# Optimization experiments

Measured on AMD Instinct MI355X. Metric: run time of the kernel, lower is better.

## Reference

```python
import jax, jax.numpy as jnp
import numpy as np

N = 6144
IN_DIM = 512
CHANNELS = 4
C_DIM = 64
ITERATIONS = 3
BETA = 1.0
EDGE_P = 0.005  # ~30 avg degree


def _l2norm(x):
    # F.normalize(dim=-1): x / max(||x||_2, eps)
    return x / jnp.maximum(jnp.linalg.norm(x, axis=-1, keepdims=True), 1e-12)


def setup_inputs() -> dict:
    key = jax.random.key(0)
    kf, ka, kw, kb = jax.random.split(key, 4)
    features = jax.random.normal(kf, (N, IN_DIM), dtype=jnp.float32)
    # sparse 0/1 adjacency, densified (module calls adj.to_dense())
    adj = (jax.random.uniform(ka, (N, N)) < EDGE_P).astype(jnp.int32)
    # per-channel weights/biases, init ~ N(0, 1) as in init_parameters
    W = jax.random.normal(kw, (CHANNELS, IN_DIM, C_DIM), dtype=jnp.float32)
    b = jax.random.normal(kb, (CHANNELS, 1, C_DIM), dtype=jnp.float32)
    return {"features": features, "adj": adj, "W": W, "b": b}


def reference(features, adj, W, b):
    mask = adj > 0  # [N, N]
    # per-channel projection + row L2-normalize -> [C, N, K]
    feats = _l2norm(jnp.einsum('nd,cdk->cnk', features, W) + b)
    for _ in range(ITERATIONS):
        # per-channel dense self-attention scores, masked by adjacency
        att = jnp.einsum('cnk,cmk->cnm', feats, feats) / BETA  # [C, N, N]
        att = jnp.where(mask[None, :, :], att, 0.0)
        # softmax across channels (torch dim=2 after cat == channel axis)
        att = jax.nn.softmax(att, axis=0)
        att = jnp.where(mask[None, :, :], att, 0.0)
        # aggregate and renormalize
        feats = _l2norm(feats + jnp.einsum('cnm,cmk->cnk', att, feats))
    # concat channels along feature dim -> [N, C*K]
    return jnp.transpose(feats, (1, 0, 2)).reshape(N, CHANNELS * C_DIM)
```

## Files before the change

### kernel.cpp

```cpp
#include <hip/hip_runtime.h>
#include <hip/hip_bf16.h>
#include <math.h>

#define NN      6144
#define IN_DIM  512
#define CH      4
#define CDIM    64
#define NODE    (CH * CDIM)
#define PR      16
#define MAXD    96

__global__ __launch_bounds__(256) void proj_kernel(
    const float* __restrict__ feat,
    const float* __restrict__ W,
    const float* __restrict__ bias,
    float* __restrict__ out)
{
    __shared__ float lds[PR * IN_DIM];
    const int t    = threadIdx.x;
    const int row0 = blockIdx.x * PR;

    {
        const float4* src = (const float4*)(feat + (size_t)row0 * IN_DIM);
        float4* dst = (float4*)lds;
#pragma unroll
        for (int i = 0; i < (PR * IN_DIM / 4) / 256; ++i)
            dst[t + i * 256] = src[t + i * 256];
    }
    __syncthreads();

    const int g  = t >> 6;
    const int q  = t & 63;
    const int c  = q >> 4;
    const int k0 = (q & 15) * 4;

    float acc[4][4];
#pragma unroll
    for (int r = 0; r < 4; ++r)
#pragma unroll
        for (int j = 0; j < 4; ++j) acc[r][j] = 0.0f;

    const float* Wc   = W + (size_t)c * IN_DIM * CDIM + k0;
    const float* arow = lds + g * 4 * IN_DIM;

    for (int d = 0; d < IN_DIM; d += 4) {
        const float4 w0 = *(const float4*)(Wc + (size_t)(d + 0) * CDIM);
        const float4 w1 = *(const float4*)(Wc + (size_t)(d + 1) * CDIM);
        const float4 w2 = *(const float4*)(Wc + (size_t)(d + 2) * CDIM);
        const float4 w3 = *(const float4*)(Wc + (size_t)(d + 3) * CDIM);
#pragma unroll
        for (int r = 0; r < 4; ++r) {
            const float4 a = *(const float4*)(arow + r * IN_DIM + d);
            acc[r][0] = fmaf(a.x, w0.x, fmaf(a.y, w1.x, fmaf(a.z, w2.x, fmaf(a.w, w3.x, acc[r][0]))));
            acc[r][1] = fmaf(a.x, w0.y, fmaf(a.y, w1.y, fmaf(a.z, w2.y, fmaf(a.w, w3.y, acc[r][1]))));
            acc[r][2] = fmaf(a.x, w0.z, fmaf(a.y, w1.z, fmaf(a.z, w2.z, fmaf(a.w, w3.z, acc[r][2]))));
            acc[r][3] = fmaf(a.x, w0.w, fmaf(a.y, w1.w, fmaf(a.z, w2.w, fmaf(a.w, w3.w, acc[r][3]))));
        }
    }

    const float4 bv = *(const float4*)(bias + c * CDIM + k0);
#pragma unroll
    for (int r = 0; r < 4; ++r) {
        acc[r][0] += bv.x; acc[r][1] += bv.y; acc[r][2] += bv.z; acc[r][3] += bv.w;
    }

    float4 res[4];
#pragma unroll
    for (int r = 0; r < 4; ++r) {
        float ss = acc[r][0] * acc[r][0] + acc[r][1] * acc[r][1]
                 + acc[r][2] * acc[r][2] + acc[r][3] * acc[r][3];
        ss += __shfl_xor(ss, 1, 64);
        ss += __shfl_xor(ss, 2, 64);
        ss += __shfl_xor(ss, 4, 64);
        ss += __shfl_xor(ss, 8, 64);
        const float rn = 1.0f / fmaxf(sqrtf(ss), 1e-12f);
        res[r] = make_float4(acc[r][0] * rn, acc[r][1] * rn, acc[r][2] * rn, acc[r][3] * rn);
    }
#pragma unroll
    for (int r = 0; r < 4; ++r) {
        *(float4*)(out + (size_t)(row0 + g * 4 + r) * NODE + c * CDIM + k0) = res[r];
    }
}

__global__ __launch_bounds__(256) void ell_kernel(
    const int* __restrict__ adj,
    int* __restrict__ deg,
    int* __restrict__ cols)
{
    __shared__ int cnt;
    const int n = blockIdx.x;
    if (threadIdx.x == 0) cnt = 0;
    __syncthreads();

    const int4* row = (const int4*)(adj + (size_t)n * NN);
    int* rowcols = cols + (size_t)n * MAXD;
    for (int i = threadIdx.x; i < NN / 4; i += 256) {
        const int4 v = row[i];
        if (v.x | v.y | v.z | v.w) {
            const int base = i * 4;
            if (v.x) { int p = atomicAdd(&cnt, 1); if (p < MAXD) rowcols[p] = base + 0; }
            if (v.y) { int p = atomicAdd(&cnt, 1); if (p < MAXD) rowcols[p] = base + 1; }
            if (v.z) { int p = atomicAdd(&cnt, 1); if (p < MAXD) rowcols[p] = base + 2; }
            if (v.w) { int p = atomicAdd(&cnt, 1); if (p < MAXD) rowcols[p] = base + 3; }
        }
    }
    __syncthreads();
    if (threadIdx.x == 0) deg[n] = min(cnt, MAXD);
}

__global__ __launch_bounds__(64) void iter_kernel(
    const float* __restrict__ fin,
    float* __restrict__ fout,
    const int* __restrict__ deg,
    const int* __restrict__ cols)
{
    const int n    = blockIdx.x;
    const int lane = threadIdx.x;

    const float4* fin4 = (const float4*)fin;
    const float4 q = fin4[(size_t)n * 64 + lane];
    float4 acc = q;

    const int d = deg[n];
    const int* cl = cols + (size_t)n * MAXD;

    int i = 0;
    for (; i + 2 <= d; i += 2) {
        const int m0 = cl[i];
        const int m1 = cl[i + 1];
        const float4 f0 = fin4[(size_t)m0 * 64 + lane];
        const float4 f1 = fin4[(size_t)m1 * 64 + lane];

        float p0 = fmaf(q.x, f0.x, fmaf(q.y, f0.y, fmaf(q.z, f0.z, q.w * f0.w)));
        float p1 = fmaf(q.x, f1.x, fmaf(q.y, f1.y, fmaf(q.z, f1.z, q.w * f1.w)));
        p0 += __shfl_xor(p0, 1, 64);  p1 += __shfl_xor(p1, 1, 64);
        p0 += __shfl_xor(p0, 2, 64);  p1 += __shfl_xor(p1, 2, 64);
        p0 += __shfl_xor(p0, 4, 64);  p1 += __shfl_xor(p1, 4, 64);
        p0 += __shfl_xor(p0, 8, 64);  p1 += __shfl_xor(p1, 8, 64);
        const float a1 = __shfl_xor(p0, 16, 64);
        const float b1 = __shfl_xor(p1, 16, 64);
        const float a2 = __shfl_xor(p0, 32, 64);
        const float b2 = __shfl_xor(p1, 32, 64);
        const float a3 = __shfl_xor(a1, 32, 64);
        const float b3 = __shfl_xor(b1, 32, 64);

        const float e0 = __expf(p0);
        const float g0 = __expf(p1);
        const float w0 = e0 / (e0 + __expf(a1) + __expf(a2) + __expf(a3));
        const float w1 = g0 / (g0 + __expf(b1) + __expf(b2) + __expf(b3));

        acc.x = fmaf(w0, f0.x, fmaf(w1, f1.x, acc.x));
        acc.y = fmaf(w0, f0.y, fmaf(w1, f1.y, acc.y));
        acc.z = fmaf(w0, f0.z, fmaf(w1, f1.z, acc.z));
        acc.w = fmaf(w0, f0.w, fmaf(w1, f1.w, acc.w));
    }
    if (i < d) {
        const int m = cl[i];
        const float4 f = fin4[(size_t)m * 64 + lane];
        float p = fmaf(q.x, f.x, fmaf(q.y, f.y, fmaf(q.z, f.z, q.w * f.w)));
        p += __shfl_xor(p, 1, 64);
        p += __shfl_xor(p, 2, 64);
        p += __shfl_xor(p, 4, 64);
        p += __shfl_xor(p, 8, 64);
        const float t1 = __shfl_xor(p, 16, 64);
        const float t2 = __shfl_xor(p, 32, 64);
        const float t3 = __shfl_xor(t1, 32, 64);
        const float e0 = __expf(p);
        const float w  = e0 / (e0 + __expf(t1) + __expf(t2) + __expf(t3));
        acc.x = fmaf(w, f.x, acc.x);
        acc.y = fmaf(w, f.y, acc.y);
        acc.z = fmaf(w, f.z, acc.z);
        acc.w = fmaf(w, f.w, acc.w);
    }

    float ss = fmaf(acc.x, acc.x, fmaf(acc.y, acc.y, fmaf(acc.z, acc.z, acc.w * acc.w)));
    ss += __shfl_xor(ss, 1, 64);
    ss += __shfl_xor(ss, 2, 64);
    ss += __shfl_xor(ss, 4, 64);
    ss += __shfl_xor(ss, 8, 64);
    const float rn = 1.0f / fmaxf(sqrtf(ss), 1e-12f);
    acc.x *= rn; acc.y *= rn; acc.z *= rn; acc.w *= rn;

    ((float4*)fout)[(size_t)n * 64 + lane] = acc;
}

extern "C" void kernel_launch(void* const* d_in, const int* in_sizes, int n_in,
                              void* d_out, int out_size, void* d_ws, size_t ws_size,
                              hipStream_t stream) {
    const float* features = (const float*)d_in[0];
    const int*   adj      = (const int*)d_in[1];
    const float* W        = (const float*)d_in[2];
    const float* b        = (const float*)d_in[3];
    float* out = (float*)d_out;

    float* featsA = (float*)d_ws;
    float* featsB = featsA + (size_t)NN * NODE;
    int*   deg    = (int*)(featsB + (size_t)NN * NODE);
    int*   cols   = deg + NN;

    proj_kernel<<<NN / PR, 256, 0, stream>>>(features, W, b, featsA);
    ell_kernel<<<NN, 256, 0, stream>>>(adj, deg, cols);
    iter_kernel<<<NN, 64, 0, stream>>>(featsA, featsB, deg, cols);
    iter_kernel<<<NN, 64, 0, stream>>>(featsB, featsA, deg, cols);
    iter_kernel<<<NN, 64, 0, stream>>>(featsA, out, deg, cols);
}
```

Measured before the change: 341.2 us.

## Prefetch neighbour rows four at a time and pack four nodes per block

The aggregation kernel now handles neighbours in groups of four. It loads the next group's column indices and feature rows before computing on the current group, so gather latency overlaps with the dot products and softmax. Each 256-thread block now serves four nodes, one per wavefront, instead of one 64-thread block per node. The channel softmax computes one exp per lane and sums it with shuffles, using hardware rcp/rsq approximations instead of division and sqrt. The dense adjacency scan now uses nontemporal loads. The cost is higher register pressure from the prefetch buffers and slightly less precise reciprocal and rsqrt results.

```diff
diff --git a/kernel.cpp b/kernel.cpp
--- a/kernel.cpp
+++ b/kernel.cpp
@@ -9,6 +9,8 @@
 #define NODE    (CH * CDIM)
 #define PR      16
 #define MAXD    96
+
+typedef int  v4i __attribute__((ext_vector_type(4)));
 
 __global__ __launch_bounds__(256) void proj_kernel(
     const float* __restrict__ feat,
@@ -64,7 +66,6 @@
         acc[r][0] += bv.x; acc[r][1] += bv.y; acc[r][2] += bv.z; acc[r][3] += bv.w;
     }
 
-    float4 res[4];
 #pragma unroll
     for (int r = 0; r < 4; ++r) {
         float ss = acc[r][0] * acc[r][0] + acc[r][1] * acc[r][1]
@@ -73,12 +74,9 @@
         ss += __shfl_xor(ss, 2, 64);
         ss += __shfl_xor(ss, 4, 64);
         ss += __shfl_xor(ss, 8, 64);
-        const float rn = 1.0f / fmaxf(sqrtf(ss), 1e-12f);
-        res[r] = make_float4(acc[r][0] * rn, acc[r][1] * rn, acc[r][2] * rn, acc[r][3] * rn);
-    }
-#pragma unroll
-    for (int r = 0; r < 4; ++r) {
-        *(float4*)(out + (size_t)(row0 + g * 4 + r) * NODE + c * CDIM + k0) = res[r];
+        const float rn = __builtin_amdgcn_rsqf(fmaxf(ss, 1e-24f));
+        float4 res = make_float4(acc[r][0] * rn, acc[r][1] * rn, acc[r][2] * rn, acc[r][3] * rn);
+        *(float4*)(out + (size_t)(row0 + g * 4 + r) * NODE + c * CDIM + k0) = res;
     }
 }
 
@@ -92,10 +90,10 @@
     if (threadIdx.x == 0) cnt = 0;
     __syncthreads();
 
-    const int4* row = (const int4*)(adj + (size_t)n * NN);
+    const v4i* row = (const v4i*)(adj + (size_t)n * NN);
     int* rowcols = cols + (size_t)n * MAXD;
     for (int i = threadIdx.x; i < NN / 4; i += 256) {
-        const int4 v = row[i];
+        const v4i v = __builtin_nontemporal_load(&row[i]);
         if (v.x | v.y | v.z | v.w) {
             const int base = i * 4;
             if (v.x) { int p = atomicAdd(&cnt, 1); if (p < MAXD) rowcols[p] = base + 0; }
@@ -108,14 +106,15 @@
     if (threadIdx.x == 0) deg[n] = min(cnt, MAXD);
 }
 
-__global__ __launch_bounds__(64) void iter_kernel(
+__global__ __launch_bounds__(256) void iter_kernel(
     const float* __restrict__ fin,
     float* __restrict__ fout,
     const int* __restrict__ deg,
     const int* __restrict__ cols)
 {
-    const int n    = blockIdx.x;
-    const int lane = threadIdx.x;
+    const int wv   = threadIdx.x >> 6;
+    const int lane = threadIdx.x & 63;
+    const int n    = blockIdx.x * 4 + wv;
 
     const float4* fin4 = (const float4*)fin;
     const float4 q = fin4[(size_t)n * 64 + lane];
@@ -123,38 +122,67 @@
 
     const int d = deg[n];
     const int* cl = cols + (size_t)n * MAXD;
-
-    int i = 0;
-    for (; i + 2 <= d; i += 2) {
-        const int m0 = cl[i];
-        const int m1 = cl[i + 1];
-        const float4 f0 = fin4[(size_t)m0 * 64 + lane];
-        const float4 f1 = fin4[(size_t)m1 * 64 + lane];
+    const int nch = d >> 2;
+
+    int4   mm;
+    float4 f0, f1, f2, f3;
+    if (nch > 0) {
+        mm = *(const int4*)cl;
+        f0 = fin4[(size_t)mm.x * 64 + lane];
+        f1 = fin4[(size_t)mm.y * 64 + lane];
+        f2 = fin4[(size_t)mm.z * 64 + lane];
+        f3 = fin4[(size_t)mm.w * 64 + lane];
+    }
+
+    for (int ch = 0; ch < nch; ++ch) {
+        int4   mn;
+        float4 g0, g1, g2, g3;
+        const bool more = (ch + 1 < nch);
+        if (more) {
+            mn = *(const int4*)(cl + (ch + 1) * 4);
+            g0 = fin4[(size_t)mn.x * 64 + lane];
+            g1 = fin4[(size_t)mn.y * 64 + lane];
+            g2 = fin4[(size_t)mn.z * 64 + lane];
+            g3 = fin4[(size_t)mn.w * 64 + lane];
+        }
 
         float p0 = fmaf(q.x, f0.x, fmaf(q.y, f0.y, fmaf(q.z, f0.z, q.w * f0.w)));
         float p1 = fmaf(q.x, f1.x, fmaf(q.y, f1.y, fmaf(q.z, f1.z, q.w * f1.w)));
-        p0 += __shfl_xor(p0, 1, 64);  p1 += __shfl_xor(p1, 1, 64);
-        p0 += __shfl_xor(p0, 2, 64);  p1 += __shfl_xor(p1, 2, 64);
-        p0 += __shfl_xor(p0, 4, 64);  p1 += __shfl_xor(p1, 4, 64);
-        p0 += __shfl_xor(p0, 8, 64);  p1 += __shfl_xor(p1, 8, 64);
-        const float a1 = __shfl_xor(p0, 16, 64);
-        const float b1 = __shfl_xor(p1, 16, 64);
-        const float a2 = __shfl_xor(p0, 32, 64);
-        const float b2 = __shfl_xor(p1, 32, 64);
-        const float a3 = __shfl_xor(a1, 32, 64);
-        const float b3 = __shfl_xor(b1, 32, 64);
-
+        float p2 = fmaf(q.x, f2.x, fmaf(q.y, f2.y, fmaf(q.z, f2.z, q.w * f2.w)));
+        float p3 = fmaf(q.x, f3.x, fmaf(q.y, f3.y, fmaf(q.z, f3.z, q.w * f3.w)));
+#pragma unroll
+        for (int off = 1; off <= 8; off <<= 1) {
+            p0 += __shfl_xor(p0, off, 64);
+            p1 += __shfl_xor(p1, off, 64);
+            p2 += __shfl_xor(p2, off, 64);
+            p3 += __shfl_xor(p3, off, 64);
+        }
         const float e0 = __expf(p0);
-        const float g0 = __expf(p1);
-        const float w0 = e0 / (e0 + __expf(a1) + __expf(a2) + __expf(a3));
-        const float w1 = g0 / (g0 + __expf(b1) + __expf(b2) + __expf(b3));
-
-        acc.x = fmaf(w0, f0.x, fmaf(w1, f1.x, acc.x));
-        acc.y = fmaf(w0, f0.y, fmaf(w1, f1.y, acc.y));
-        acc.z = fmaf(w0, f0.z, fmaf(w1, f1.z, acc.z));
-        acc.w = fmaf(w0, f0.w, fmaf(w1, f1.w, acc.w));
-    }
-    if (i < d) {
+        const float e1 = __expf(p1);
+        const float e2 = __expf(p2);
+        const float e3 = __expf(p3);
+        float s0 = e0 + __shfl_xor(e0, 16, 64);
+        float s1 = e1 + __shfl_xor(e1, 16, 64);
+        float s2 = e2 + __shfl_xor(e2, 16, 64);
+        float s3 = e3 + __shfl_xor(e3, 16, 64);
+        s0 += __shfl_xor(s0, 32, 64);
+        s1 += __shfl_xor(s1, 32, 64);
+        s2 += __shfl_xor(s2, 32, 64);
+        s3 += __shfl_xor(s3, 32, 64);
+        const float w0 = e0 * __builtin_amdgcn_rcpf(s0);
+        const float w1 = e1 * __builtin_amdgcn_rcpf(s1);
+        const float w2 = e2 * __builtin_amdgcn_rcpf(s2);
+        const float w3 = e3 * __builtin_amdgcn_rcpf(s3);
+
+        acc.x = fmaf(w0, f0.x, fmaf(w1, f1.x, fmaf(w2, f2.x, fmaf(w3, f3.x, acc.x))));
+        acc.y = fmaf(w0, f0.y, fmaf(w1, f1.y, fmaf(w2, f2.y, fmaf(w3, f3.y, acc.y))));
+        acc.z = fmaf(w0, f0.z, fmaf(w1, f1.z, fmaf(w2, f2.z, fmaf(w3, f3.z, acc.z))));
+        acc.w = fmaf(w0, f0.w, fmaf(w1, f1.w, fmaf(w2, f2.w, fmaf(w3, f3.w, acc.w))));
+
+        if (more) { f0 = g0; f1 = g1; f2 = g2; f3 = g3; }
+    }
+
+    for (int i = nch * 4; i < d; ++i) {
         const int m = cl[i];
         const float4 f = fin4[(size_t)m * 64 + lane];
         float p = fmaf(q.x, f.x, fmaf(q.y, f.y, fmaf(q.z, f.z, q.w * f.w)));
@@ -162,11 +190,10 @@
         p += __shfl_xor(p, 2, 64);
         p += __shfl_xor(p, 4, 64);
         p += __shfl_xor(p, 8, 64);
-        const float t1 = __shfl_xor(p, 16, 64);
-        const float t2 = __shfl_xor(p, 32, 64);
-        const float t3 = __shfl_xor(t1, 32, 64);
-        const float e0 = __expf(p);
-        const float w  = e0 / (e0 + __expf(t1) + __expf(t2) + __expf(t3));
+        const float e = __expf(p);
+        float s = e + __shfl_xor(e, 16, 64);
+        s += __shfl_xor(s, 32, 64);
+        const float w = e * __builtin_amdgcn_rcpf(s);
         acc.x = fmaf(w, f.x, acc.x);
         acc.y = fmaf(w, f.y, acc.y);
         acc.z = fmaf(w, f.z, acc.z);
@@ -178,7 +205,7 @@
     ss += __shfl_xor(ss, 2, 64);
     ss += __shfl_xor(ss, 4, 64);
     ss += __shfl_xor(ss, 8, 64);
-    const float rn = 1.0f / fmaxf(sqrtf(ss), 1e-12f);
+    const float rn = __builtin_amdgcn_rsqf(fmaxf(ss, 1e-24f));
     acc.x *= rn; acc.y *= rn; acc.z *= rn; acc.w *= rn;
 
     ((float4*)fout)[(size_t)n * 64 + lane] = acc;
@@ -200,7 +227,7 @@
 
     proj_kernel<<<NN / PR, 256, 0, stream>>>(features, W, b, featsA);
     ell_kernel<<<NN, 256, 0, stream>>>(adj, deg, cols);
-    iter_kernel<<<NN, 64, 0, stream>>>(featsA, featsB, deg, cols);
-    iter_kernel<<<NN, 64, 0, stream>>>(featsB, featsA, deg, cols);
-    iter_kernel<<<NN, 64, 0, stream>>>(featsA, out, deg, cols);
-}
+    iter_kernel<<<NN / 4, 256, 0, stream>>>(featsA, featsB, deg, cols);
+    iter_kernel<<<NN / 4, 256, 0, stream>>>(featsB, featsA, deg, cols);
+    iter_kernel<<<NN / 4, 256, 0, stream>>>(featsA, out, deg, cols);
+}
```

New measurement: 319.8 us. 1.07x faster.
